# Performance work log

Measured on AMD Instinct MI355X. Metric: run time of the kernel, lower is better.

The kernel has to match this reference:

```python
import jax, jax.numpy as jnp
import numpy as np

B, S, HID = 1, 8192, 768
H, D = 12, 64          # num heads, head dim (HID = H*D)
W = 256                # one-sided attention window


def _shift_chunks(xc, C):
    # xc: [B, C, w, H, D] -> prev/next chunk copies padded with zeros
    prev = jnp.pad(xc, ((0, 0), (1, 0), (0, 0), (0, 0), (0, 0)))[:, :C]
    nxt = jnp.pad(xc, ((0, 0), (0, 1), (0, 0), (0, 0), (0, 0)))[:, 1:]
    return jnp.concatenate([prev, xc, nxt], axis=2)  # [B, C, 3w, H, D]


def sliding_window_attention(q, k, v, w):
    # q,k,v: [B, S, H, D]; q already scaled. Band width 2w+1.
    b, s, h, d = q.shape
    c = s // w
    qc = q.reshape(b, c, w, h, d)
    k3 = _shift_chunks(k.reshape(b, c, w, h, d), c)  # [b,c,3w,h,d]
    v3 = _shift_chunks(v.reshape(b, c, w, h, d), c)
    # scores of each query chunk against its 3-chunk key neighborhood
    scores3 = jnp.einsum('bcxhd,bcyhd->bhcxy', qc, k3)  # [b,h,c,w,3w]
    rows = jnp.arange(w)
    offs = jnp.arange(2 * w + 1)
    gidx = rows[:, None] + offs[None, :]  # [w, 2w+1] local key index p+j
    band = scores3[..., rows[:, None], gidx]  # [b,h,c,w,2w+1]
    # mask keys outside [0, S) (same effect as mask_invalid_locations)
    gq = jnp.arange(s).reshape(c, w)                    # global query pos
    keypos = gq[..., None] + (offs - w)                 # [c,w,2w+1]
    valid = (keypos >= 0) & (keypos < s)
    band = jnp.where(valid[None, None], band, -jnp.inf)
    prob = jax.nn.softmax(band, axis=-1)
    prob = jnp.where(valid[None, None], prob, 0.0)
    # scatter band probs back to 3w layout, then banded PV matmul
    prob3 = jnp.zeros(band.shape[:-1] + (3 * w,), band.dtype)
    prob3 = prob3.at[..., rows[:, None], gidx].set(prob)  # [b,h,c,w,3w]
    ctx = jnp.einsum('bhcxy,bcyhd->bcxhd', prob3, v3)
    return ctx.reshape(b, s, h, d)


def setup_inputs() -> dict:
    key = jax.random.key(0)
    ks = jax.random.split(key, 4)
    sc = 1.0 / np.sqrt(HID)
    return {
        'hidden_states': jax.random.normal(ks[0], (B, S, HID), jnp.float32),
        'Wq': jax.random.normal(ks[1], (HID, HID), jnp.float32) * sc,
        'bq': jnp.zeros((HID,), jnp.float32),
        'Wk': jax.random.normal(ks[2], (HID, HID), jnp.float32) * sc,
        'bk': jnp.zeros((HID,), jnp.float32),
        'Wv': jax.random.normal(ks[3], (HID, HID), jnp.float32) * sc,
        'bv': jnp.zeros((HID,), jnp.float32),
    }


def reference(hidden_states, Wq, bq, Wk, bk, Wv, bv):
    b, s, hid = hidden_states.shape
    q = (hidden_states @ Wq + bq).reshape(b, s, H, D)
    k = (hidden_states @ Wk + bk).reshape(b, s, H, D)
    v = (hidden_states @ Wv + bv).reshape(b, s, H, D)
    q = q / jnp.asarray(np.sqrt(D), q.dtype)
    ctx = sliding_window_attention(q, k, v, W)  # [b,s,H,D]
    return ctx.reshape(b, s, hid)
```

## Files before the change

kernel.cpp:

```cpp
#include <hip/hip_runtime.h>
#include <hip/hip_bf16.h>

#define S_LEN 8192
#define HID 768
#define NH 12
#define HD 64
#define WIN 256

typedef __bf16 bf16x8 __attribute__((ext_vector_type(8)));
typedef float f32x4 __attribute__((ext_vector_type(4)));
using bf16_t = __hip_bfloat16;

#define MFMA(a, b, c) __builtin_amdgcn_mfma_f32_16x16x32_bf16(a, b, c, 0, 0, 0)

__device__ __forceinline__ void gl2lds16(const bf16_t* g, bf16_t* l) {
  __builtin_amdgcn_global_load_lds(
      (const __attribute__((address_space(1))) void*)g,
      (__attribute__((address_space(3))) void*)l, 16, 0, 0);
}

__global__ __launch_bounds__(256) void prep(const float* __restrict__ hs,
                                            bf16_t* __restrict__ hb,
                                            const float* __restrict__ Wq,
                                            const float* __restrict__ Wk,
                                            const float* __restrict__ Wv,
                                            bf16_t* __restrict__ Wt) {
  int bx = blockIdx.x;
  int tid = threadIdx.x;
  if (bx < 6144) {
    int i = (bx * 256 + tid) * 4;
    float4 v = *reinterpret_cast<const float4*>(hs + i);
    union { ushort4 u; bf16_t b[4]; } H;
    H.b[0] = __float2bfloat16(v.x);
    H.b[1] = __float2bfloat16(v.y);
    H.b[2] = __float2bfloat16(v.z);
    H.b[3] = __float2bfloat16(v.w);
    *reinterpret_cast<ushort4*>(hb + i) = H.u;
    return;
  }
  __shared__ float t[32][33];
  int b = bx - 6144;
  int z = b / 576;
  int r = b % 576;
  int n0 = (r / 24) * 32, k0 = (r % 24) * 32;
  const float* src = (z == 0) ? Wq : ((z == 1) ? Wk : Wv);
  int tx = tid & 31, ty = tid >> 5;
  for (int i = 0; i < 4; ++i)
    t[ty + i * 8][tx] = src[(k0 + ty + i * 8) * HID + n0 + tx];
  __syncthreads();
  bf16_t* dst = Wt + z * HID * HID;
  for (int i = 0; i < 4; ++i)
    dst[(n0 + ty + i * 8) * HID + k0 + tx] = __float2bfloat16(t[tx][ty + i * 8]);
}

__global__ __launch_bounds__(256) void qkv_gemm(
    const bf16_t* __restrict__ hb, const bf16_t* __restrict__ Wt,
    const float* __restrict__ bq, const float* __restrict__ bk,
    const float* __restrict__ bv,
    bf16_t* __restrict__ Qw, bf16_t* __restrict__ Kw, bf16_t* __restrict__ Vt) {
  __shared__ __align__(16) bf16_t sA[128 * 64];
  __shared__ __align__(16) bf16_t sB[128 * 64];
  int m0 = blockIdx.x * 128;
  int zq = blockIdx.y / 6;
  int nn0 = (blockIdx.y % 6) * 128;
  int n0g = zq * HID + nn0;
  int tid = threadIdx.x;
  int w = tid >> 6, lane = tid & 63, lm = lane & 15, qd = lane >> 4;
  int wm = w & 1, wn = w >> 1;

  int srow = w * 8 + (lane >> 3);
  int sc8 = (lane & 7) ^ ((lane >> 3) & 7);
  const bf16_t* gA = hb + (m0 + srow) * HID + sc8 * 8;
  const bf16_t* gB = Wt + (n0g + srow) * HID + sc8 * 8;
  int sx0 = lm & 7;

  f32x4 acc[4][4] = {};
  for (int kk = 0; kk < HID; kk += 64) {
#pragma unroll
    for (int u = 0; u < 4; ++u) {
      gl2lds16(gA + (u * 32) * HID + kk, sA + u * 2048 + w * 512);
      gl2lds16(gB + (u * 32) * HID + kk, sB + u * 2048 + w * 512);
    }
    __syncthreads();
#pragma unroll
    for (int half = 0; half < 2; ++half) {
      int ca = (qd + 4 * half) ^ sx0;
      bf16x8 fa[4], fb[4];
#pragma unroll
      for (int i = 0; i < 4; ++i) {
        fa[i] = *reinterpret_cast<const bf16x8*>(
            sA + (wm * 64 + i * 16 + lm) * 64 + ca * 8);
        fb[i] = *reinterpret_cast<const bf16x8*>(
            sB + (wn * 64 + i * 16 + lm) * 64 + ca * 8);
      }
      if (zq == 2) {
#pragma unroll
        for (int i = 0; i < 4; ++i)
#pragma unroll
          for (int j = 0; j < 4; ++j)
            acc[i][j] = MFMA(fb[i], fa[j], acc[i][j]);
      } else {
#pragma unroll
        for (int i = 0; i < 4; ++i)
#pragma unroll
          for (int j = 0; j < 4; ++j)
            acc[i][j] = MFMA(fa[i], fb[j], acc[i][j]);
      }
    }
    __syncthreads();
  }

  if (zq != 2) {
    const float* bias = zq ? bk : bq;
    bf16_t* dst = zq ? Kw : Qw;
    float scale = zq ? 1.0f : 0.125f;
#pragma unroll
    for (int j = 0; j < 4; ++j) {
      int nl = nn0 + wn * 64 + j * 16 + lm;
      float bb = bias[nl];
      int h = nl >> 6, d = nl & 63;
#pragma unroll
      for (int i = 0; i < 4; ++i)
#pragma unroll
        for (int r = 0; r < 4; ++r) {
          int m = m0 + wm * 64 + i * 16 + qd * 4 + r;
          dst[(h * S_LEN + m) * HD + d] =
              __float2bfloat16((acc[i][j][r] + bb) * scale);
        }
    }
  } else {
#pragma unroll
    for (int i = 0; i < 4; ++i)
#pragma unroll
      for (int r = 0; r < 4; ++r) {
        int nl = nn0 + wn * 64 + i * 16 + qd * 4 + r;
        float bb = bv[nl];
#pragma unroll
        for (int j = 0; j < 4; ++j) {
          int m = m0 + wm * 64 + j * 16 + lm;
          Vt[nl * S_LEN + m] = __float2bfloat16(acc[i][j][r] + bb);
        }
      }
  }
}

__global__ __launch_bounds__(256, 4) void swa_kernel(
    const bf16_t* __restrict__ Qw, const bf16_t* __restrict__ Kw,
    const bf16_t* __restrict__ Vt, float* __restrict__ out) {
  __shared__ __align__(16) bf16_t sK[2][64 * 64];
  __shared__ __align__(16) bf16_t sV[2][64 * 64];
  __shared__ __align__(16) bf16_t sP[4 * 16 * 64];
  int h = blockIdx.y;
  int nb = blockIdx.x;
  int q0 = (((nb & 7) << 4) | (nb >> 3)) * 64;
  int tid = threadIdx.x;
  int w = tid >> 6, lane = tid & 63, lm = lane & 15, qd = lane >> 4;
  int xb = q0 + w * 16;

  int qoff = (h * S_LEN + xb + lm) * HD + qd * 8;
  bf16x8 aq0 = *reinterpret_cast<const bf16x8*>(Qw + qoff);
  bf16x8 aq1 = *reinterpret_cast<const bf16x8*>(Qw + qoff + 32);

  f32x4 o[4] = {};
  float lsum = 0.f;

  int y_begin = q0 - WIN; if (y_begin < 0) y_begin = 0;
  int y_end = q0 + 64 + WIN; if (y_end > S_LEN) y_end = S_LEN;
  int ntiles = (y_end - y_begin) >> 6;
  const bf16_t* Kh = Kw + h * S_LEN * HD;
  const bf16_t* Vh = Vt + h * HD * S_LEN;
  bf16_t* sPw = sP + w * 16 * 64;

  int srow = w * 8 + (lane >> 3);
  int sc8 = (lane & 7) ^ ((lane >> 3) & 7);
  int sx0 = lm & 7;

#define STAGE(y0, b)                                                    \
  {                                                                     \
    const bf16_t* kg = Kh + ((y0) + srow) * HD + sc8 * 8;               \
    gl2lds16(kg, &sK[b][w * 512]);                                      \
    gl2lds16(kg + 32 * HD, &sK[b][2048 + w * 512]);                     \
    const bf16_t* vg = Vh + srow * S_LEN + (y0) + sc8 * 8;              \
    gl2lds16(vg, &sV[b][w * 512]);                                      \
    gl2lds16(vg + 32 * S_LEN, &sV[b][2048 + w * 512]);                  \
  }

  STAGE(y_begin, 0);
  __syncthreads();

  for (int t = 0; t < ntiles; ++t) {
    int y0 = y_begin + t * 64;
    if (t + 1 < ntiles) STAGE(y0 + 64, (t + 1) & 1);
    int b = t & 1;
    f32x4 s[4] = {};
#pragma unroll
    for (int nt = 0; nt < 4; ++nt) {
      const bf16_t* kr = &sK[b][(nt * 16 + lm) * 64];
      bf16x8 b0 = *reinterpret_cast<const bf16x8*>(kr + (qd ^ sx0) * 8);
      bf16x8 b1 = *reinterpret_cast<const bf16x8*>(kr + ((qd + 4) ^ sx0) * 8);
      s[nt] = MFMA(b0, aq0, s[nt]);
      s[nt] = MFMA(b1, aq1, s[nt]);
    }
    int dy = y0 - q0;
    bool edge = (dy > 192) || (dy < -192);
#pragma unroll
    for (int nt = 0; nt < 4; ++nt) {
      union { ushort4 u; bf16_t b[4]; } P;
#pragma unroll
      for (int r = 0; r < 4; ++r) {
        float pv;
        if (edge) {
          int dlt = (y0 + nt * 16 + qd * 4 + r) - (xb + lm);
          pv = (dlt <= WIN && dlt >= -WIN) ? __expf(s[nt][r]) : 0.f;
        } else {
          pv = __expf(s[nt][r]);
        }
        lsum += pv;
        P.b[r] = __float2bfloat16(pv);
      }
      *reinterpret_cast<ushort4*>(
          sPw + lm * 64 + (((2 * nt + (qd >> 1)) ^ sx0) * 8) + (qd & 1) * 4) =
          P.u;
    }
    bf16x8 ap0 =
        *reinterpret_cast<const bf16x8*>(sPw + lm * 64 + ((qd ^ sx0) * 8));
    bf16x8 ap1 = *reinterpret_cast<const bf16x8*>(sPw + lm * 64 +
                                                  (((qd + 4) ^ sx0) * 8));
#pragma unroll
    for (int nt = 0; nt < 4; ++nt) {
      const bf16_t* vr = &sV[b][(nt * 16 + lm) * 64];
      bf16x8 v0 = *reinterpret_cast<const bf16x8*>(vr + (qd ^ sx0) * 8);
      bf16x8 v1 = *reinterpret_cast<const bf16x8*>(vr + ((qd + 4) ^ sx0) * 8);
      o[nt] = MFMA(ap0, v0, o[nt]);
      o[nt] = MFMA(ap1, v1, o[nt]);
    }
    __syncthreads();
  }
  lsum += __shfl_xor(lsum, 16);
  lsum += __shfl_xor(lsum, 32);
#pragma unroll
  for (int r = 0; r < 4; ++r) {
    float inv = 1.f / __shfl(lsum, qd * 4 + r);
    int x = xb + qd * 4 + r;
#pragma unroll
    for (int nt = 0; nt < 4; ++nt)
      out[x * HID + h * HD + nt * 16 + lm] = o[nt][r] * inv;
  }
}

extern "C" void kernel_launch(void* const* d_in, const int* in_sizes, int n_in,
                              void* d_out, int out_size, void* d_ws, size_t ws_size,
                              hipStream_t stream) {
  const float* hs = (const float*)d_in[0];
  const float* Wq = (const float*)d_in[1];
  const float* bq = (const float*)d_in[2];
  const float* Wk = (const float*)d_in[3];
  const float* bk = (const float*)d_in[4];
  const float* Wv = (const float*)d_in[5];
  const float* bv = (const float*)d_in[6];
  float* out = (float*)d_out;

  const int NSH = S_LEN * HID;
  const int NW = 3 * HID * HID;
  bf16_t* p = (bf16_t*)d_ws;
  bf16_t* hb = p; p += NSH;
  bf16_t* Wt = p; p += NW;
  bf16_t* Qw = p; p += NSH;
  bf16_t* Kw = p; p += NSH;
  bf16_t* Vt = p; p += NSH;

  prep<<<dim3(6144 + 1728), dim3(256), 0, stream>>>(hs, hb, Wq, Wk, Wv, Wt);
  qkv_gemm<<<dim3(64, 18), dim3(256), 0, stream>>>(
      hb, Wt, bq, bk, bv, Qw, Kw, Vt);
  swa_kernel<<<dim3(128, 12), dim3(256), 0, stream>>>(Qw, Kw, Vt, out);
}
```

Baseline: 166.2 us.

## Triple-buffer QKV GEMM with 512-thread 128x256 tiles and interleaved prefetch

The QKV projection GEMM now uses 512-thread blocks computing 128x256 output tiles, with a three-stage LDS ring buffer so global-to-LDS loads for step t+2 run while MFMAs consume step t. A and B prefetches are split across the two k-halves, ordered with explicit vmcnt waits and raw barriers, and the MFMA phases get raised scheduling priority. The goal is to hide memory latency and halve the per-iteration syncthreads stalls of the old single-buffered loop. The cost is much more LDS per block, which limits occupancy, and hand-written waitcnt logic that must match the load counts exactly.

```diff
diff --git a/kernel.cpp b/kernel.cpp
--- a/kernel.cpp
+++ b/kernel.cpp
@@ -53,20 +53,20 @@
     dst[(n0 + ty + i * 8) * HID + k0 + tx] = __float2bfloat16(t[tx][ty + i * 8]);
 }
 
-__global__ __launch_bounds__(256) void qkv_gemm(
+__global__ __launch_bounds__(512, 2) void qkv_gemm(
     const bf16_t* __restrict__ hb, const bf16_t* __restrict__ Wt,
     const float* __restrict__ bq, const float* __restrict__ bk,
     const float* __restrict__ bv,
     bf16_t* __restrict__ Qw, bf16_t* __restrict__ Kw, bf16_t* __restrict__ Vt) {
-  __shared__ __align__(16) bf16_t sA[128 * 64];
-  __shared__ __align__(16) bf16_t sB[128 * 64];
+  __shared__ __align__(16) bf16_t sA[3][128 * 64];
+  __shared__ __align__(16) bf16_t sB[3][256 * 64];
   int m0 = blockIdx.x * 128;
-  int zq = blockIdx.y / 6;
-  int nn0 = (blockIdx.y % 6) * 128;
+  int zq = blockIdx.y / 3;
+  int nn0 = (blockIdx.y % 3) * 256;
   int n0g = zq * HID + nn0;
   int tid = threadIdx.x;
   int w = tid >> 6, lane = tid & 63, lm = lane & 15, qd = lane >> 4;
-  int wm = w & 1, wn = w >> 1;
+  int wm = w >> 2, wn = w & 3;
 
   int srow = w * 8 + (lane >> 3);
   int sc8 = (lane & 7) ^ ((lane >> 3) & 7);
@@ -74,40 +74,78 @@
   const bf16_t* gB = Wt + (n0g + srow) * HID + sc8 * 8;
   int sx0 = lm & 7;
 
+#define STAGE_A(kk, bb)                                      \
+  {                                                          \
+    gl2lds16(gA + (kk), &sA[bb][w * 512]);                   \
+    gl2lds16(gA + 64 * HID + (kk), &sA[bb][4096 + w * 512]); \
+  }
+#define STAGE_B(kk, bb)                                        \
+  {                                                            \
+    gl2lds16(gB + (kk), &sB[bb][w * 512]);                     \
+    gl2lds16(gB + 64 * HID + (kk), &sB[bb][4096 + w * 512]);   \
+    gl2lds16(gB + 128 * HID + (kk), &sB[bb][8192 + w * 512]);  \
+    gl2lds16(gB + 192 * HID + (kk), &sB[bb][12288 + w * 512]); \
+  }
+
+#define PHASE_MFMA(FA, FB)                                \
+  __builtin_amdgcn_s_setprio(1);                          \
+  if (zq == 2) {                                          \
+    _Pragma("unroll") for (int i = 0; i < 4; ++i)         \
+        _Pragma("unroll") for (int j = 0; j < 4; ++j)     \
+            acc[i][j] = MFMA(FB[i], FA[j], acc[i][j]);    \
+  } else {                                                \
+    _Pragma("unroll") for (int i = 0; i < 4; ++i)         \
+        _Pragma("unroll") for (int j = 0; j < 4; ++j)     \
+            acc[i][j] = MFMA(FA[i], FB[j], acc[i][j]);    \
+  }                                                       \
+  __builtin_amdgcn_s_setprio(0);
+
+  STAGE_A(0, 0); STAGE_B(0, 0);
+  STAGE_A(64, 1); STAGE_B(64, 1);
+  asm volatile("s_waitcnt vmcnt(6)" ::: "memory");
+  __builtin_amdgcn_s_barrier();
+
   f32x4 acc[4][4] = {};
-  for (int kk = 0; kk < HID; kk += 64) {
-#pragma unroll
-    for (int u = 0; u < 4; ++u) {
-      gl2lds16(gA + (u * 32) * HID + kk, sA + u * 2048 + w * 512);
-      gl2lds16(gB + (u * 32) * HID + kk, sB + u * 2048 + w * 512);
-    }
-    __syncthreads();
-#pragma unroll
-    for (int half = 0; half < 2; ++half) {
-      int ca = (qd + 4 * half) ^ sx0;
+  for (int t = 0; t < 12; ++t) {
+    const bf16_t* a_c = sA[t % 3];
+    const bf16_t* b_c = sB[t % 3];
+    int nb = (t + 2) % 3;
+    int kk2 = (t + 2) * 64;
+    {
       bf16x8 fa[4], fb[4];
+      int ca = qd ^ sx0;
 #pragma unroll
       for (int i = 0; i < 4; ++i) {
         fa[i] = *reinterpret_cast<const bf16x8*>(
-            sA + (wm * 64 + i * 16 + lm) * 64 + ca * 8);
+            a_c + (wm * 64 + i * 16 + lm) * 64 + ca * 8);
         fb[i] = *reinterpret_cast<const bf16x8*>(
-            sB + (wn * 64 + i * 16 + lm) * 64 + ca * 8);
-      }
-      if (zq == 2) {
-#pragma unroll
-        for (int i = 0; i < 4; ++i)
-#pragma unroll
-          for (int j = 0; j < 4; ++j)
-            acc[i][j] = MFMA(fb[i], fa[j], acc[i][j]);
-      } else {
-#pragma unroll
-        for (int i = 0; i < 4; ++i)
-#pragma unroll
-          for (int j = 0; j < 4; ++j)
-            acc[i][j] = MFMA(fa[i], fb[j], acc[i][j]);
-      }
-    }
-    __syncthreads();
+            b_c + (wn * 64 + i * 16 + lm) * 64 + ca * 8);
+      }
+      if (t < 10) STAGE_A(kk2, nb);
+      __builtin_amdgcn_s_barrier();
+      PHASE_MFMA(fa, fb);
+      __builtin_amdgcn_s_barrier();
+    }
+    {
+      bf16x8 fa[4], fb[4];
+      int ca = (qd + 4) ^ sx0;
+#pragma unroll
+      for (int i = 0; i < 4; ++i) {
+        fa[i] = *reinterpret_cast<const bf16x8*>(
+            a_c + (wm * 64 + i * 16 + lm) * 64 + ca * 8);
+        fb[i] = *reinterpret_cast<const bf16x8*>(
+            b_c + (wn * 64 + i * 16 + lm) * 64 + ca * 8);
+      }
+      if (t < 10) STAGE_B(kk2, nb);
+      __builtin_amdgcn_s_barrier();
+      PHASE_MFMA(fa, fb);
+      if (t < 10) {
+        asm volatile("s_waitcnt vmcnt(6)" ::: "memory");
+      } else if (t < 11) {
+        asm volatile("s_waitcnt vmcnt(0)" ::: "memory");
+      }
+      __builtin_amdgcn_s_barrier();
+    }
   }
 
   if (zq != 2) {
@@ -270,7 +308,7 @@
   bf16_t* Vt = p; p += NSH;
 
   prep<<<dim3(6144 + 1728), dim3(256), 0, stream>>>(hs, hb, Wq, Wk, Wv, Wt);
-  qkv_gemm<<<dim3(64, 18), dim3(256), 0, stream>>>(
+  qkv_gemm<<<dim3(64, 9), dim3(512), 0, stream>>>(
       hb, Wt, bq, bk, bv, Qw, Kw, Vt);
   swa_kernel<<<dim3(128, 12), dim3(256), 0, stream>>>(Qw, Kw, Vt, out);
 }
```

Result: slower. 176.0 us (+5.9%).
